# Kernel tuning notes

Measured on AMD Instinct MI355X. Metric: run time of the kernel, lower is better.

## Reference

```python
import jax, jax.numpy as jnp
import numpy as np

B, S, H, D, HID = 2, 4096, 16, 64, 1024
NUM_HASHES, CHUNK, NUM_BUCKETS = 2, 64, 128
N_BEFORE, N_AFTER = 1, 0
HASH_SEED = 0
SELF_MASK_VALUE = -1e5  # fp32 self-mask value from source buffers
EPS = 1e-6


def _look_adjacent(x, n_before, n_after):
    # x: [B,H,C,chunk,...]; concat chunks rolled along chunk axis (2) onto within-chunk axis (3)
    slices = [jnp.roll(x, -i, axis=2) for i in range(-n_before, n_after + 1)]
    return jnp.concatenate(slices, axis=3)


def _hash_vectors(vectors, rotations, num_buckets):
    # vectors: [B,H,S,D]; rotations: [H,D,NUM_HASHES,num_buckets//2] (shared q/k, seed reset in source)
    v = jax.lax.stop_gradient(vectors)  # vectors.detach() in source
    rotated = jnp.einsum('bhsd,hdnr->bhnsr', v, rotations)
    rotated = jnp.concatenate([rotated, -rotated], axis=-1)
    buckets = jnp.argmax(rotated, axis=-1)  # [B,H,NUM_HASHES,S]
    offsets = (jnp.arange(NUM_HASHES) * num_buckets).reshape(1, 1, -1, 1)
    return (buckets + offsets).reshape(vectors.shape[0], H, -1)  # [B,H,NUM_HASHES*S]


def _sorted_and_undo(buckets, seq_len):
    orig = jnp.arange(NUM_HASHES * seq_len) % seq_len
    scaled = seq_len * buckets + orig  # stable within-bucket ordering by position
    sorted_idx = jnp.argsort(scaled, axis=-1)
    undo_idx = jnp.argsort(sorted_idx, axis=-1)  # scatter-inverse of the sort
    return sorted_idx, undo_idx


def _len_and_dim_norm(x):
    var = jnp.mean(x * x, axis=-1, keepdims=True)
    return x * jax.lax.rsqrt(var + EPS) * np.float32(1.0 / np.sqrt(D))


def setup_inputs() -> dict:
    key = jax.random.key(0)
    k1, k2, k3, k4 = jax.random.split(key, 4)
    return {
        'decoder_states': jax.random.normal(k1, (B, S, HID), jnp.float32),
        'hidden_states': jax.random.normal(k2, (B, S, HID), jnp.float32),
        'w_qk': jax.random.normal(k3, (HID, H * D), jnp.float32) / np.float32(np.sqrt(HID)),
        'w_v': jax.random.normal(k4, (HID, H * D), jnp.float32) / np.float32(np.sqrt(HID)),
    }


def reference(decoder_states, hidden_states, w_qk, w_v):
    # projections (bias-free, Reformer-style), split heads -> [B,H,S,D]
    q = (decoder_states @ w_qk).reshape(B, S, H, D).transpose(0, 2, 1, 3)
    k = (hidden_states @ w_qk).reshape(B, S, H, D).transpose(0, 2, 1, 3)
    v = (hidden_states @ w_v).reshape(B, S, H, D).transpose(0, 2, 1, 3)

    rotations = jax.random.normal(jax.random.key(HASH_SEED),
                                  (H, D, NUM_HASHES, NUM_BUCKETS // 2), jnp.float32)
    q_buckets = _hash_vectors(q, rotations, NUM_BUCKETS)
    k_buckets = _hash_vectors(k, rotations, NUM_BUCKETS)
    sorted_q_idx, _ = _sorted_and_undo(q_buckets, S)
    sorted_k_idx, undo_k_idx = _sorted_and_undo(k_buckets, S)
    sorted_q_pos = sorted_q_idx % S
    sorted_k_pos = sorted_k_idx % S

    gather = lambda x, idx: jnp.take_along_axis(x, idx[..., None], axis=2)
    qs = gather(q, sorted_q_pos)  # [B,H,NUM_HASHES*S,D]
    ks = gather(k, sorted_k_pos)
    vs = gather(v, sorted_k_pos)

    n_chunks = NUM_HASHES * S // CHUNK
    to_chunks = lambda x: x.reshape(B, H, n_chunks, CHUNK, D)
    qs, ks, vs = to_chunks(qs), to_chunks(ks), to_chunks(vs)
    ks = _len_and_dim_norm(ks)

    ks = _look_adjacent(ks, N_BEFORE, N_AFTER)  # [B,H,C,2*CHUNK,D]
    vs = _look_adjacent(vs, N_BEFORE, N_AFTER)
    dots = jnp.einsum('bhcqd,bhckd->bhcqk', qs, ks)

    # self-mask: query position == adjacent key position (both from sorted QUERY idx, per source)
    q_idx = sorted_q_pos.reshape(B, H, n_chunks, CHUNK)
    kv_idx = _look_adjacent(q_idx, N_BEFORE, N_AFTER)  # [B,H,C,2*CHUNK]
    self_mask = q_idx[..., :, None] != kv_idx[..., None, :]
    dots = jnp.where(self_mask, dots, SELF_MASK_VALUE)

    logits = jax.nn.logsumexp(dots, axis=-1, keepdims=True)
    probs = jnp.exp(dots - logits)
    out = jnp.einsum('bhcqk,bhckd->bhcqd', probs, vs)

    out = out.reshape(B, H, NUM_HASHES * S, D)
    logits = logits.reshape(B, H, NUM_HASHES * S)
    # ReverseSort uses the KEY undo indices (as in source)
    out = jnp.take_along_axis(out, undo_k_idx[..., None], axis=2)
    logits = jnp.take_along_axis(logits, undo_k_idx, axis=2)

    # merge hash rounds via logsumexp weights (num_hashes > 1 branch)
    out = out.reshape(B, H, NUM_HASHES, S, D)
    logits = logits.reshape(B, H, NUM_HASHES, S, 1)
    w = jnp.exp(logits - jax.nn.logsumexp(logits, axis=2, keepdims=True))
    out = jnp.sum(out * w, axis=2)  # [B,H,S,D]
    return out.transpose(0, 2, 1, 3).reshape(B, S, H * D)
```

## Files before the change

kernel.cpp:

```cpp
#include <hip/hip_runtime.h>
#include <cstdint>
#include <cstddef>

#define BB 2
#define SS 4096
#define HH 16
#define DD 64
#define HID 1024
#define NHASH 2
#define CHUNK 64
#define NBUCK 128
#define NCHUNKS 128
#define NSORT 8192
#define BHN 32

#define KC_BLOCK 288

static constexpr size_t SZ_QKV  = (size_t)BB*HH*SS*DD*4;
static constexpr size_t OFF_Q   = 0;
static constexpr size_t OFF_K   = OFF_Q + SZ_QKV;
static constexpr size_t OFF_V   = OFF_K + SZ_QKV;
static constexpr size_t OFF_ROT = OFF_V + SZ_QKV;
static constexpr size_t OFF_QB  = OFF_ROT + (size_t)131072*4;
static constexpr size_t OFF_KB  = OFF_QB + (size_t)BHN*NSORT*4;
static constexpr size_t OFF_SQ  = OFF_KB + (size_t)BHN*NSORT*4;
static constexpr size_t OFF_SK  = OFF_SQ + (size_t)BHN*NSORT*4;
static constexpr size_t OFF_OUTR= OFF_SK + (size_t)BHN*NSORT*4;
static constexpr size_t OFF_LR  = OFF_OUTR + (size_t)BHN*NSORT*DD*4;
static constexpr size_t OFF_HBF = OFF_LR + (size_t)BHN*NSORT*4;
static constexpr size_t OFF_WBF = OFF_HBF + (size_t)8192*1024*2;
static constexpr size_t WS_REQUIRED = OFF_WBF + (size_t)1024*1024*2;

__device__ __forceinline__ float nofma_mul(float a, float b) {
  float r = a * b;
  asm("" : "+v"(r));
  return r;
}

__device__ __forceinline__ float xla_log1p_f32(float x) {
  float t = nofma_mul(-0.5f, x) + 1.0f;
  float small = nofma_mul(t, x);
  float onep = 1.0f + x;
  float big = (float)log((double)onep);
  return (fabsf(x) < 1e-4f) ? small : big;
}

__device__ __forceinline__ float erfinv_xla_f32(float x) {
  float nxx = -nofma_mul(x, x);
  float w = -xla_log1p_f32(nxx);
  float p;
  if (w < 5.0f) {
    float ww = w - 2.5f;
    p = 2.81022636e-08f;
    p = nofma_mul(p, ww) + 3.43273939e-07f;
    p = nofma_mul(p, ww) + -3.5233877e-06f;
    p = nofma_mul(p, ww) + -4.39150654e-06f;
    p = nofma_mul(p, ww) + 0.00021858087f;
    p = nofma_mul(p, ww) + -0.00125372503f;
    p = nofma_mul(p, ww) + -0.00417768164f;
    p = nofma_mul(p, ww) + 0.246640727f;
    p = nofma_mul(p, ww) + 1.50140941f;
  } else {
    float ww = sqrtf(w) - 3.0f;
    p = -0.000200214257f;
    p = nofma_mul(p, ww) + 0.000100950558f;
    p = nofma_mul(p, ww) + 0.00134934322f;
    p = nofma_mul(p, ww) + -0.00367342844f;
    p = nofma_mul(p, ww) + 0.00573950773f;
    p = nofma_mul(p, ww) + -0.0076224613f;
    p = nofma_mul(p, ww) + 0.00943887047f;
    p = nofma_mul(p, ww) + 1.00167406f;
    p = nofma_mul(p, ww) + 2.83297682f;
  }
  return nofma_mul(p, x);
}

__global__ void gen_rot_kernel(float* __restrict__ rot) {
  unsigned i = blockIdx.x * 256 + threadIdx.x;
  if (i >= 131072u) return;
  unsigned x0 = 0u, x1 = i;
  const unsigned ks2 = 0x1BD11BDAu;
#define TF_ROUND(r) { x0 += x1; x1 = (x1 << r) | (x1 >> (32 - r)); x1 ^= x0; }
  TF_ROUND(13) TF_ROUND(15) TF_ROUND(26) TF_ROUND(6)
              x1 += ks2 + 1u;
  TF_ROUND(17) TF_ROUND(29) TF_ROUND(16) TF_ROUND(24)
   x0 += ks2; x1 += 2u;
  TF_ROUND(13) TF_ROUND(15) TF_ROUND(26) TF_ROUND(6)
              x1 += 3u;
  TF_ROUND(17) TF_ROUND(29) TF_ROUND(16) TF_ROUND(24)
              x1 += ks2 + 4u;
  TF_ROUND(13) TF_ROUND(15) TF_ROUND(26) TF_ROUND(6)
   x0 += ks2; x1 += 5u;
#undef TF_ROUND
  unsigned bits = x0 ^ x1;
  float f = __uint_as_float(0x3f800000u | (bits >> 9)) - 1.0f;
  float u = f * 2.0f - 0.99999994f;
  u = fmaxf(-0.99999994f, u);
  rot[i] = nofma_mul(1.41421356f, erfinv_xla_f32(u));
}

__global__ __launch_bounds__(256) void gemm_kernel(const float* __restrict__ A,
                                                   const float* __restrict__ W,
                                                   float* __restrict__ dst) {
  __shared__ float As[32][132];
  __shared__ float Bs[32][68];
  const int m0 = blockIdx.x * 128;
  const int n0 = blockIdx.y * 64;
  const int tid = threadIdx.x;
  const int tr = tid >> 4, tc = tid & 15;
  float accT[8][4], acc[8][4];
#pragma unroll
  for (int i = 0; i < 8; ++i)
#pragma unroll
    for (int j2 = 0; j2 < 4; ++j2) { accT[i][j2] = 0.f; acc[i][j2] = 0.f; }

  float4 av[4], bv[2];
#pragma unroll
  for (int it = 0; it < 4; ++it) {
    int id = tid + it * 256;
    av[it] = *(const float4*)(A + (size_t)(m0 + (id >> 3)) * 1024 + ((id & 7) << 2));
  }
#pragma unroll
  for (int it = 0; it < 2; ++it) {
    int id = tid + it * 256;
    bv[it] = *(const float4*)(W + (size_t)(id >> 4) * 1024 + n0 + ((id & 15) << 2));
  }
  for (int kk = 0; kk < 1024; kk += 32) {
#pragma unroll
    for (int it = 0; it < 4; ++it) {
      int id = tid + it * 256;
      int m = id >> 3, kq = (id & 7) << 2;
      As[kq + 0][m] = av[it].x;
      As[kq + 1][m] = av[it].y;
      As[kq + 2][m] = av[it].z;
      As[kq + 3][m] = av[it].w;
    }
#pragma unroll
    for (int it = 0; it < 2; ++it) {
      int id = tid + it * 256;
      *(float4*)&Bs[id >> 4][(id & 15) << 2] = bv[it];
    }
    __syncthreads();
    if (kk + 32 < 1024) {
      int kn = kk + 32;
#pragma unroll
      for (int it = 0; it < 4; ++it) {
        int id = tid + it * 256;
        av[it] = *(const float4*)(A + (size_t)(m0 + (id >> 3)) * 1024 + kn + ((id & 7) << 2));
      }
#pragma unroll
      for (int it = 0; it < 2; ++it) {
        int id = tid + it * 256;
        bv[it] = *(const float4*)(W + (size_t)(kn + (id >> 4)) * 1024 + n0 + ((id & 15) << 2));
      }
    }
#pragma unroll
    for (int k = 0; k < 32; ++k) {
      float4 a0 = *(const float4*)&As[k][tr * 8];
      float4 a1 = *(const float4*)&As[k][tr * 8 + 4];
      float4 b0 = *(const float4*)&Bs[k][tc * 4];
      float a[8] = {a0.x, a0.y, a0.z, a0.w, a1.x, a1.y, a1.z, a1.w};
      float b[4] = {b0.x, b0.y, b0.z, b0.w};
#pragma unroll
      for (int i = 0; i < 8; ++i)
#pragma unroll
        for (int j2 = 0; j2 < 4; ++j2)
          acc[i][j2] = fmaf(a[i], b[j2], acc[i][j2]);
    }
    __syncthreads();
    if (((kk + 32) % KC_BLOCK) == 0) {
#pragma unroll
      for (int i = 0; i < 8; ++i)
#pragma unroll
        for (int j2 = 0; j2 < 4; ++j2) { accT[i][j2] += acc[i][j2]; acc[i][j2] = 0.f; }
    }
  }
#pragma unroll
  for (int i = 0; i < 8; ++i)
#pragma unroll
    for (int j2 = 0; j2 < 4; ++j2) accT[i][j2] += acc[i][j2];

  const int h = n0 >> 6;
  const int d = tc << 2;
#pragma unroll
  for (int i = 0; i < 8; ++i) {
    int m = m0 + tr * 8 + i;
    int b = m >> 12, s = m & 4095;
    float4 t = {accT[i][0], accT[i][1], accT[i][2], accT[i][3]};
    *(float4*)(dst + (((size_t)(b * 16 + h) * 4096 + s) << 6) + d) = t;
  }
}

__device__ __forceinline__ unsigned short f2bf(float f) {
  unsigned u = __float_as_uint(f);
  return (unsigned short)((u + 0x7fffu + ((u >> 16) & 1u)) >> 16);
}
__global__ void cast_bf16_kernel(const float* __restrict__ src,
                                 unsigned short* __restrict__ dst, int n4) {
  int i = blockIdx.x * 256 + threadIdx.x;
  if (i >= n4) return;
  float4 v = ((const float4*)src)[i];
  ushort4 o = {f2bf(v.x), f2bf(v.y), f2bf(v.z), f2bf(v.w)};
  ((ushort4*)dst)[i] = o;
}

typedef __attribute__((ext_vector_type(8))) short bf16x8;
typedef __attribute__((ext_vector_type(4))) float f32x4;

__global__ __launch_bounds__(256) void gemm_v_mfma(const unsigned short* __restrict__ Ab,
                                                   const unsigned short* __restrict__ Wb,
                                                   float* __restrict__ dst) {
  __shared__ unsigned short Bt[64][40];
  const int m0 = blockIdx.x * 64;
  const int n0 = blockIdx.y * 64;
  const int tid = threadIdx.x;
  const int w = tid >> 6, l = tid & 63;
  f32x4 acc[4];
#pragma unroll
  for (int fi = 0; fi < 4; ++fi) acc[fi] = {0.f, 0.f, 0.f, 0.f};

  const int arow = m0 + w * 16 + (l & 15);
  const int kgrp = (l >> 4) * 8;
  for (int kk = 0; kk < 1024; kk += 32) {
    {
      int k = tid >> 3, n8 = (tid & 7) * 8;
      bf16x8 v = *(const bf16x8*)(Wb + (size_t)(kk + k) * 1024 + n0 + n8);
#pragma unroll
      for (int i = 0; i < 8; ++i) Bt[n8 + i][k] = (unsigned short)v[i];
    }
    __syncthreads();
    bf16x8 a = *(const bf16x8*)(Ab + (size_t)arow * 1024 + kk + kgrp);
#pragma unroll
    for (int fi = 0; fi < 4; ++fi) {
      bf16x8 b = *(const bf16x8*)(&Bt[fi * 16 + (l & 15)][kgrp]);
      acc[fi] = __builtin_amdgcn_mfma_f32_16x16x32_bf16(a, b, acc[fi], 0, 0, 0);
    }
    __syncthreads();
  }
  const int h = n0 >> 6;
  const int mrow = m0 + w * 16 + (l >> 4) * 4;
#pragma unroll
  for (int fi = 0; fi < 4; ++fi) {
    int d = fi * 16 + (l & 15);
#pragma unroll
    for (int r = 0; r < 4; ++r) {
      int m = mrow + r;
      int b = m >> 12, s = m & 4095;
      dst[(((size_t)(b * 16 + h) * 4096 + s) << 6) + d] = acc[fi][r];
    }
  }
}

__global__ __launch_bounds__(128) void hash_kernel(const float* __restrict__ x,
                                                   const float* __restrict__ rot,
                                                   int* __restrict__ buck) {
  __shared__ float rs[8192];
  const int bh = blockIdx.y;
  const int h = bh & 15;
  const int s0 = blockIdx.x * 128;
  const int tid = threadIdx.x;
  for (int off = tid * 4; off < 8192; off += 512)
    *(float4*)&rs[off] = *(const float4*)(rot + (size_t)h * 8192 + off);
  __syncthreads();
  const int s = s0 + tid;
  const float* xr = x + ((size_t)bh * SS + s) * DD;
  float xv[64];
#pragma unroll
  for (int d4 = 0; d4 < 16; ++d4) {
    float4 t = *(const float4*)(xr + d4 * 4);
    xv[d4 * 4] = t.x; xv[d4 * 4 + 1] = t.y; xv[d4 * 4 + 2] = t.z; xv[d4 * 4 + 3] = t.w;
  }
#pragma unroll
  for (int n = 0; n < 2; ++n) {
    float acc[64];
#pragma unroll
    for (int r = 0; r < 64; ++r) acc[r] = 0.f;
#pragma unroll 2
    for (int d4 = 0; d4 < 16; ++d4) {
#pragma unroll
      for (int dd = 0; dd < 4; ++dd) {
        const float xd = xv[d4 * 4 + dd];
        const float* rp = rs + (d4 * 4 + dd) * 128 + n * 64;
#pragma unroll
        for (int r4 = 0; r4 < 16; ++r4) {
          float4 rv = *(const float4*)(rp + r4 * 4);
          acc[r4 * 4 + 0] = fmaf(xd, rv.x, acc[r4 * 4 + 0]);
          acc[r4 * 4 + 1] = fmaf(xd, rv.y, acc[r4 * 4 + 1]);
          acc[r4 * 4 + 2] = fmaf(xd, rv.z, acc[r4 * 4 + 2]);
          acc[r4 * 4 + 3] = fmaf(xd, rv.w, acc[r4 * 4 + 3]);
        }
      }
    }
    float best = -3.402823466e38f;
    int bi = 0;
#pragma unroll
    for (int idx = 0; idx < 128; ++idx) {
      float val = (idx < 64) ? acc[idx] : -acc[idx - 64];
      if (val > best) { best = val; bi = idx; }
    }
    buck[(size_t)bh * NSORT + n * SS + s] = bi + n * NBUCK;
  }
}

__global__ __launch_bounds__(256) void sort_kernel(const int* __restrict__ buck,
                                                   int* __restrict__ sorted) {
  const int bh = blockIdx.x >> 1;
  const int half = blockIdx.x & 1;
  const int* bk = buck + (size_t)bh * NSORT + half * SS;
  int* out = sorted + (size_t)bh * NSORT + half * SS;
  __shared__ int cnt[64][128];
  __shared__ int bl[SS];
  __shared__ int bbase[128];
  __shared__ int total[128];
  const int tid = threadIdx.x;
  for (int i = tid; i < 64 * 128; i += 256) (&cnt[0][0])[i] = 0;
  __syncthreads();
#pragma unroll
  for (int j = 0; j < 16; ++j) {
    int i = j * 256 + tid;
    int e = bk[i];
    bl[i] = e;
    atomicAdd(&cnt[i >> 6][e & 127], 1);
  }
  __syncthreads();
  if (tid < 128) {
    int s = 0;
#pragma unroll 4
    for (int c = 0; c < 64; ++c) {
      int t = cnt[c][tid];
      cnt[c][tid] = s;
      s += t;
    }
    total[tid] = s;
  }
  __syncthreads();
  if (tid == 0) {
    int s = 0;
#pragma unroll 4
    for (int v = 0; v < 128; ++v) { bbase[v] = s; s += total[v]; }
  }
  __syncthreads();
  if (tid < 64) {
    const int i0 = tid << 6;
    const int orig0 = half * SS + i0;
#pragma unroll 4
    for (int j = 0; j < 64; ++j) {
      int v = bl[i0 + j] & 127;
      int off = cnt[tid][v];
      cnt[tid][v] = off + 1;
      out[bbase[v] + off] = orig0 + j;
    }
  }
}

__global__ void undo_kernel(const int* __restrict__ srt, int* __restrict__ undo) {
  const int bh = blockIdx.x;
  for (int j = threadIdx.x; j < NSORT; j += 256)
    undo[(size_t)bh * NSORT + srt[(size_t)bh * NSORT + j]] = j;
}

__global__ __launch_bounds__(256) void attn_kernel(const float* __restrict__ q,
                                                   const float* __restrict__ k,
                                                   const float* __restrict__ v,
                                                   const int* __restrict__ sq,
                                                   const int* __restrict__ sk,
                                                   float* __restrict__ outr,
                                                   float* __restrict__ lr) {
  const int c = blockIdx.x;
  const int bh = blockIdx.y;
  const int cprev = (c + NCHUNKS - 1) & (NCHUNKS - 1);
  __shared__ float Ks[128][68];
  __shared__ float Vs[128][68];
  __shared__ int qpos[64];
  __shared__ int kvpos[128];
  __shared__ int krow[128];
  __shared__ float kscale[128];
  const int tid = threadIdx.x;
  const int* sqb = sq + (size_t)bh * NSORT;
  const int* skb = sk + (size_t)bh * NSORT;
  if (tid < 64) {
    int sqc = sqb[c * 64 + tid];
    int sqp = sqb[cprev * 64 + tid];
    qpos[tid] = sqc & (SS - 1);
    kvpos[tid] = sqp & (SS - 1);
    kvpos[64 + tid] = sqc & (SS - 1);
    int skc = skb[c * 64 + tid];
    int skp = skb[cprev * 64 + tid];
    krow[tid] = skp & (SS - 1);
    krow[64 + tid] = skc & (SS - 1);
  }
  __syncthreads();
  const float* kb = k + (size_t)bh * SS * DD;
  const float* vb = v + (size_t)bh * SS * DD;
#pragma unroll
  for (int it = 0; it < 8; ++it) {
    int id = tid + it * 256;
    int row = id >> 4, c4 = (id & 15) * 4;
    int srow = krow[row];
    *(float4*)&Ks[row][c4] = *(const float4*)(kb + (size_t)srow * DD + c4);
    *(float4*)&Vs[row][c4] = *(const float4*)(vb + (size_t)srow * DD + c4);
  }
  __syncthreads();
  if (tid < 128) {
    float ss = 0.f;
#pragma unroll
    for (int c4 = 0; c4 < 16; ++c4) {
      float4 t = *(const float4*)&Ks[tid][c4 * 4];
      ss += t.x * t.x + t.y * t.y + t.z * t.z + t.w * t.w;
    }
    kscale[tid] = rsqrtf(ss * (1.f / 64.f) + 1e-6f) * 0.125f;
  }
  __syncthreads();

  const int qi = tid >> 2, g = tid & 3;
  const int qp = qpos[qi];
  const float* qrow = q + ((size_t)bh * SS + qp) * DD;
  float qreg[64];
#pragma unroll
  for (int d4 = 0; d4 < 16; ++d4) {
    float4 t = *(const float4*)(qrow + d4 * 4);
    qreg[d4 * 4] = t.x; qreg[d4 * 4 + 1] = t.y; qreg[d4 * 4 + 2] = t.z; qreg[d4 * 4 + 3] = t.w;
  }
  float dots[32];
#pragma unroll
  for (int j = 0; j < 32; ++j) {
    const int kj = j * 4 + g;
    float acc = 0.f;
#pragma unroll
    for (int d4 = 0; d4 < 16; ++d4) {
      float4 t = *(const float4*)&Ks[kj][d4 * 4];
      acc = fmaf(qreg[d4 * 4 + 0], t.x, acc);
      acc = fmaf(qreg[d4 * 4 + 1], t.y, acc);
      acc = fmaf(qreg[d4 * 4 + 2], t.z, acc);
      acc = fmaf(qreg[d4 * 4 + 3], t.w, acc);
    }
    acc *= kscale[kj];
    if (qp == kvpos[kj]) acc = -1e5f;
    dots[j] = acc;
  }
  float m = dots[0];
#pragma unroll
  for (int j = 1; j < 32; ++j) m = fmaxf(m, dots[j]);
  m = fmaxf(m, __shfl_xor(m, 1));
  m = fmaxf(m, __shfl_xor(m, 2));
  float se = 0.f;
#pragma unroll
  for (int j = 0; j < 32; ++j) { dots[j] = expf(dots[j] - m); se += dots[j]; }
  se += __shfl_xor(se, 1);
  se += __shfl_xor(se, 2);
  const float logit = m + logf(se);
  const float seinv = 1.f / se;
  float o[64];
#pragma unroll
  for (int d = 0; d < 64; ++d) o[d] = 0.f;
#pragma unroll
  for (int j = 0; j < 32; ++j) {
    const int kj = j * 4 + g;
    const float p = dots[j] * seinv;
#pragma unroll
    for (int d4 = 0; d4 < 16; ++d4) {
      float4 t = *(const float4*)&Vs[kj][d4 * 4];
      o[d4 * 4 + 0] = fmaf(p, t.x, o[d4 * 4 + 0]);
      o[d4 * 4 + 1] = fmaf(p, t.y, o[d4 * 4 + 1]);
      o[d4 * 4 + 2] = fmaf(p, t.z, o[d4 * 4 + 2]);
      o[d4 * 4 + 3] = fmaf(p, t.w, o[d4 * 4 + 3]);
    }
  }
#pragma unroll
  for (int d = 0; d < 64; ++d) {
    o[d] += __shfl_xor(o[d], 1);
    o[d] += __shfl_xor(o[d], 2);
  }
  float* orow = outr + ((size_t)bh * NSORT + c * 64 + qi) * DD;
#pragma unroll
  for (int d4 = 0; d4 < 4; ++d4) {
    float4 t = {o[g * 16 + d4 * 4], o[g * 16 + d4 * 4 + 1], o[g * 16 + d4 * 4 + 2], o[g * 16 + d4 * 4 + 3]};
    *(float4*)(orow + g * 16 + d4 * 4) = t;
  }
  if (g == 0) lr[(size_t)bh * NSORT + c * 64 + qi] = logit;
}

__global__ void merge_kernel(const float* __restrict__ outr, const float* __restrict__ lr,
                             const int* __restrict__ undo, float* __restrict__ out) {
  const int idx = blockIdx.x * 256 + threadIdx.x;
  const int d4 = idx & 15;
  const int s = (idx >> 4) & (SS - 1);
  const int bh = idx >> 16;
  const int b = bh >> 4, h = bh & 15;
  const int u0 = undo[(size_t)bh * NSORT + s];
  const int u1 = undo[(size_t)bh * NSORT + SS + s];
  const float l0 = lr[(size_t)bh * NSORT + u0];
  const float l1 = lr[(size_t)bh * NSORT + u1];
  const float m = fmaxf(l0, l1);
  float w0 = expf(l0 - m), w1 = expf(l1 - m);
  const float inv = 1.f / (w0 + w1);
  w0 *= inv; w1 *= inv;
  const float4 r0 = *(const float4*)(outr + ((size_t)bh * NSORT + u0) * DD + d4 * 4);
  const float4 r1 = *(const float4*)(outr + ((size_t)bh * NSORT + u1) * DD + d4 * 4);
  float4 o;
  o.x = w0 * r0.x + w1 * r1.x;
  o.y = w0 * r0.y + w1 * r1.y;
  o.z = w0 * r0.z + w1 * r1.z;
  o.w = w0 * r0.w + w1 * r1.w;
  *(float4*)(out + ((size_t)(b * SS + s) * 1024) + h * 64 + d4 * 4) = o;
}

extern "C" void kernel_launch(void* const* d_in, const int* in_sizes, int n_in,
                              void* d_out, int out_size, void* d_ws, size_t ws_size,
                              hipStream_t stream) {
  if (ws_size < WS_REQUIRED) return;
  const float* dec = (const float*)d_in[0];
  const float* hid = (const float*)d_in[1];
  const float* wqk = (const float*)d_in[2];
  const float* wv  = (const float*)d_in[3];
  float* out = (float*)d_out;
  char* ws = (char*)d_ws;
  float* q    = (float*)(ws + OFF_Q);
  float* kk   = (float*)(ws + OFF_K);
  float* vv   = (float*)(ws + OFF_V);
  float* rotp = (float*)(ws + OFF_ROT);
  int*   qb   = (int*)(ws + OFF_QB);
  int*   kbk  = (int*)(ws + OFF_KB);
  int*   sqi  = (int*)(ws + OFF_SQ);
  int*   ski  = (int*)(ws + OFF_SK);
  float* outr = (float*)(ws + OFF_OUTR);
  float* lrp  = (float*)(ws + OFF_LR);
  unsigned short* hbf = (unsigned short*)(ws + OFF_HBF);
  unsigned short* wbf = (unsigned short*)(ws + OFF_WBF);

  gen_rot_kernel<<<512, 256, 0, stream>>>(rotp);
  cast_bf16_kernel<<<8192, 256, 0, stream>>>(hid, hbf, 8192 * 1024 / 4);
  cast_bf16_kernel<<<1024, 256, 0, stream>>>(wv, wbf, 1024 * 1024 / 4);
  gemm_kernel<<<dim3(64, 16), 256, 0, stream>>>(dec, wqk, q);
  gemm_kernel<<<dim3(64, 16), 256, 0, stream>>>(hid, wqk, kk);
  gemm_v_mfma<<<dim3(128, 16), 256, 0, stream>>>(hbf, wbf, vv);
  hash_kernel<<<dim3(32, 32), 128, 0, stream>>>(q, rotp, qb);
  hash_kernel<<<dim3(32, 32), 128, 0, stream>>>(kk, rotp, kbk);
  sort_kernel<<<64, 256, 0, stream>>>(qb, sqi);
  sort_kernel<<<64, 256, 0, stream>>>(kbk, ski);
  undo_kernel<<<32, 256, 0, stream>>>(ski, qb);
  attn_kernel<<<dim3(128, 32), 256, 0, stream>>>(q, kk, vv, sqi, ski, outr, lrp);
  merge_kernel<<<8192, 256, 0, stream>>>(outr, lrp, qb, out);
}
```

Baseline: 0.9996 ms.

## Rewrite chunked attention with bf16 MFMA for QK^T and PV

The scalar fp32 attention kernel is replaced by one that stages Q, K and transposed V in shared memory as bf16 and computes QK^T and P·V with 16x16x32 bf16 MFMA instructions. Softmax row reductions now run across lanes in the MFMA output layout, and the probabilities go through shared memory as bf16. V is now written as bf16 by the V GEMM, and Q and K get two extra cast kernels. This cuts FP32 ALU work and the bandwidth of the K/V gathers, at the cost of bf16 rounding in the scores, the probabilities and the key norm.

```diff
diff --git a/kernel.cpp b/kernel.cpp
--- a/kernel.cpp
+++ b/kernel.cpp
@@ -29,7 +29,9 @@
 static constexpr size_t OFF_LR  = OFF_OUTR + (size_t)BHN*NSORT*DD*4;
 static constexpr size_t OFF_HBF = OFF_LR + (size_t)BHN*NSORT*4;
 static constexpr size_t OFF_WBF = OFF_HBF + (size_t)8192*1024*2;
-static constexpr size_t WS_REQUIRED = OFF_WBF + (size_t)1024*1024*2;
+static constexpr size_t OFF_QBF = OFF_WBF + (size_t)1024*1024*2;
+static constexpr size_t OFF_KBF = OFF_QBF + (size_t)BHN*SS*DD*2;
+static constexpr size_t WS_REQUIRED = OFF_KBF + (size_t)BHN*SS*DD*2;
 
 __device__ __forceinline__ float nofma_mul(float a, float b) {
   float r = a * b;
@@ -209,7 +211,7 @@
 
 __global__ __launch_bounds__(256) void gemm_v_mfma(const unsigned short* __restrict__ Ab,
                                                    const unsigned short* __restrict__ Wb,
-                                                   float* __restrict__ dst) {
+                                                   unsigned short* __restrict__ dst) {
   __shared__ unsigned short Bt[64][40];
   const int m0 = blockIdx.x * 64;
   const int n0 = blockIdx.y * 64;
@@ -246,7 +248,7 @@
     for (int r = 0; r < 4; ++r) {
       int m = mrow + r;
       int b = m >> 12, s = m & 4095;
-      dst[(((size_t)(b * 16 + h) * 4096 + s) << 6) + d] = acc[fi][r];
+      dst[(((size_t)(b * 16 + h) * 4096 + s) << 6) + d] = f2bf(acc[fi][r]);
     }
   }
 }
@@ -359,18 +361,17 @@
     undo[(size_t)bh * NSORT + srt[(size_t)bh * NSORT + j]] = j;
 }
 
-__global__ __launch_bounds__(256) void attn_kernel(const float* __restrict__ q,
-                                                   const float* __restrict__ k,
-                                                   const float* __restrict__ v,
-                                                   const int* __restrict__ sq,
-                                                   const int* __restrict__ sk,
-                                                   float* __restrict__ outr,
-                                                   float* __restrict__ lr) {
-  const int c = blockIdx.x;
-  const int bh = blockIdx.y;
+__global__ __launch_bounds__(256) void attn_mfma_kernel(
+    const unsigned short* __restrict__ qb16, const unsigned short* __restrict__ kb16,
+    const unsigned short* __restrict__ vb16,
+    const int* __restrict__ sq, const int* __restrict__ sk,
+    float* __restrict__ outr, float* __restrict__ lr) {
+  const int c = blockIdx.x, bh = blockIdx.y;
   const int cprev = (c + NCHUNKS - 1) & (NCHUNKS - 1);
-  __shared__ float Ks[128][68];
-  __shared__ float Vs[128][68];
+  __shared__ unsigned short Qs[64][80];
+  __shared__ unsigned short Ks[128][80];
+  __shared__ unsigned short Vt[64][136];
+  __shared__ unsigned short Ps[64][136];
   __shared__ int qpos[64];
   __shared__ int kvpos[128];
   __shared__ int krow[128];
@@ -384,100 +385,122 @@
     qpos[tid] = sqc & (SS - 1);
     kvpos[tid] = sqp & (SS - 1);
     kvpos[64 + tid] = sqc & (SS - 1);
-    int skc = skb[c * 64 + tid];
-    int skp = skb[cprev * 64 + tid];
-    krow[tid] = skp & (SS - 1);
-    krow[64 + tid] = skc & (SS - 1);
-  }
-  __syncthreads();
-  const float* kb = k + (size_t)bh * SS * DD;
-  const float* vb = v + (size_t)bh * SS * DD;
-#pragma unroll
-  for (int it = 0; it < 8; ++it) {
+    krow[tid] = skb[cprev * 64 + tid] & (SS - 1);
+    krow[64 + tid] = skb[c * 64 + tid] & (SS - 1);
+  }
+  __syncthreads();
+  const unsigned short* kbase = kb16 + (size_t)bh * SS * DD;
+  const unsigned short* vbase = vb16 + (size_t)bh * SS * DD;
+  const unsigned short* qbase = qb16 + (size_t)bh * SS * DD;
+#pragma unroll
+  for (int it = 0; it < 4; ++it) {
     int id = tid + it * 256;
-    int row = id >> 4, c4 = (id & 15) * 4;
-    int srow = krow[row];
-    *(float4*)&Ks[row][c4] = *(const float4*)(kb + (size_t)srow * DD + c4);
-    *(float4*)&Vs[row][c4] = *(const float4*)(vb + (size_t)srow * DD + c4);
+    int row = id >> 3, seg = id & 7;
+    *(bf16x8*)&Ks[row][seg * 8] = *(const bf16x8*)(kbase + (size_t)krow[row] * DD + seg * 8);
+  }
+#pragma unroll
+  for (int it = 0; it < 2; ++it) {
+    int id = tid + it * 256;
+    int row = id >> 3, seg = id & 7;
+    *(bf16x8*)&Qs[row][seg * 8] = *(const bf16x8*)(qbase + (size_t)qpos[row] * DD + seg * 8);
+  }
+#pragma unroll
+  for (int it = 0; it < 4; ++it) {
+    int id = tid + it * 256;
+    int col = id & 127, dg = id >> 7;
+    bf16x8 v = *(const bf16x8*)(vbase + (size_t)krow[col] * DD + dg * 8);
+#pragma unroll
+    for (int i = 0; i < 8; ++i) Vt[dg * 8 + i][col] = (unsigned short)v[i];
   }
   __syncthreads();
   if (tid < 128) {
     float ss = 0.f;
 #pragma unroll
-    for (int c4 = 0; c4 < 16; ++c4) {
-      float4 t = *(const float4*)&Ks[tid][c4 * 4];
-      ss += t.x * t.x + t.y * t.y + t.z * t.z + t.w * t.w;
+    for (int seg = 0; seg < 8; ++seg) {
+      bf16x8 t = *(const bf16x8*)&Ks[tid][seg * 8];
+#pragma unroll
+      for (int i = 0; i < 8; ++i) {
+        float f = __uint_as_float(((unsigned)(unsigned short)t[i]) << 16);
+        ss = fmaf(f, f, ss);
+      }
     }
     kscale[tid] = rsqrtf(ss * (1.f / 64.f) + 1e-6f) * 0.125f;
   }
   __syncthreads();
 
-  const int qi = tid >> 2, g = tid & 3;
-  const int qp = qpos[qi];
-  const float* qrow = q + ((size_t)bh * SS + qp) * DD;
-  float qreg[64];
-#pragma unroll
-  for (int d4 = 0; d4 < 16; ++d4) {
-    float4 t = *(const float4*)(qrow + d4 * 4);
-    qreg[d4 * 4] = t.x; qreg[d4 * 4 + 1] = t.y; qreg[d4 * 4 + 2] = t.z; qreg[d4 * 4 + 3] = t.w;
-  }
-  float dots[32];
-#pragma unroll
-  for (int j = 0; j < 32; ++j) {
-    const int kj = j * 4 + g;
-    float acc = 0.f;
-#pragma unroll
-    for (int d4 = 0; d4 < 16; ++d4) {
-      float4 t = *(const float4*)&Ks[kj][d4 * 4];
-      acc = fmaf(qreg[d4 * 4 + 0], t.x, acc);
-      acc = fmaf(qreg[d4 * 4 + 1], t.y, acc);
-      acc = fmaf(qreg[d4 * 4 + 2], t.z, acc);
-      acc = fmaf(qreg[d4 * 4 + 3], t.w, acc);
-    }
-    acc *= kscale[kj];
-    if (qp == kvpos[kj]) acc = -1e5f;
-    dots[j] = acc;
-  }
-  float m = dots[0];
-#pragma unroll
-  for (int j = 1; j < 32; ++j) m = fmaxf(m, dots[j]);
-  m = fmaxf(m, __shfl_xor(m, 1));
-  m = fmaxf(m, __shfl_xor(m, 2));
-  float se = 0.f;
-#pragma unroll
-  for (int j = 0; j < 32; ++j) { dots[j] = expf(dots[j] - m); se += dots[j]; }
-  se += __shfl_xor(se, 1);
-  se += __shfl_xor(se, 2);
-  const float logit = m + logf(se);
-  const float seinv = 1.f / se;
-  float o[64];
-#pragma unroll
-  for (int d = 0; d < 64; ++d) o[d] = 0.f;
-#pragma unroll
-  for (int j = 0; j < 32; ++j) {
-    const int kj = j * 4 + g;
-    const float p = dots[j] * seinv;
-#pragma unroll
-    for (int d4 = 0; d4 < 16; ++d4) {
-      float4 t = *(const float4*)&Vs[kj][d4 * 4];
-      o[d4 * 4 + 0] = fmaf(p, t.x, o[d4 * 4 + 0]);
-      o[d4 * 4 + 1] = fmaf(p, t.y, o[d4 * 4 + 1]);
-      o[d4 * 4 + 2] = fmaf(p, t.z, o[d4 * 4 + 2]);
-      o[d4 * 4 + 3] = fmaf(p, t.w, o[d4 * 4 + 3]);
-    }
-  }
-#pragma unroll
-  for (int d = 0; d < 64; ++d) {
-    o[d] += __shfl_xor(o[d], 1);
-    o[d] += __shfl_xor(o[d], 2);
-  }
-  float* orow = outr + ((size_t)bh * NSORT + c * 64 + qi) * DD;
-#pragma unroll
-  for (int d4 = 0; d4 < 4; ++d4) {
-    float4 t = {o[g * 16 + d4 * 4], o[g * 16 + d4 * 4 + 1], o[g * 16 + d4 * 4 + 2], o[g * 16 + d4 * 4 + 3]};
-    *(float4*)(orow + g * 16 + d4 * 4) = t;
-  }
-  if (g == 0) lr[(size_t)bh * NSORT + c * 64 + qi] = logit;
+  const int w = tid >> 6, l = tid & 63;
+  const int lc = l & 15, lg = l >> 4;
+  bf16x8 a0 = *(const bf16x8*)&Qs[w * 16 + lc][lg * 8];
+  bf16x8 a1 = *(const bf16x8*)&Qs[w * 16 + lc][32 + lg * 8];
+  f32x4 accs[8];
+#pragma unroll
+  for (int fi = 0; fi < 8; ++fi) {
+    f32x4 acc = {0.f, 0.f, 0.f, 0.f};
+    bf16x8 b0 = *(const bf16x8*)&Ks[fi * 16 + lc][lg * 8];
+    bf16x8 b1 = *(const bf16x8*)&Ks[fi * 16 + lc][32 + lg * 8];
+    acc = __builtin_amdgcn_mfma_f32_16x16x32_bf16(a0, b0, acc, 0, 0, 0);
+    acc = __builtin_amdgcn_mfma_f32_16x16x32_bf16(a1, b1, acc, 0, 0, 0);
+    accs[fi] = acc;
+  }
+  float kcs[8]; int kvp[8];
+#pragma unroll
+  for (int fi = 0; fi < 8; ++fi) { kcs[fi] = kscale[fi * 16 + lc]; kvp[fi] = kvpos[fi * 16 + lc]; }
+  float ex[8][4], logit_r[4], seinv_r[4];
+#pragma unroll
+  for (int r = 0; r < 4; ++r) {
+    const int qp = qpos[w * 16 + lg * 4 + r];
+    float mr = -3.402823466e38f;
+#pragma unroll
+    for (int fi = 0; fi < 8; ++fi) {
+      float d = accs[fi][r] * kcs[fi];
+      if (qp == kvp[fi]) d = -1e5f;
+      ex[fi][r] = d;
+      mr = fmaxf(mr, d);
+    }
+    mr = fmaxf(mr, __shfl_xor(mr, 1));
+    mr = fmaxf(mr, __shfl_xor(mr, 2));
+    mr = fmaxf(mr, __shfl_xor(mr, 4));
+    mr = fmaxf(mr, __shfl_xor(mr, 8));
+    float s = 0.f;
+#pragma unroll
+    for (int fi = 0; fi < 8; ++fi) { float e = expf(ex[fi][r] - mr); ex[fi][r] = e; s += e; }
+    s += __shfl_xor(s, 1);
+    s += __shfl_xor(s, 2);
+    s += __shfl_xor(s, 4);
+    s += __shfl_xor(s, 8);
+    logit_r[r] = mr + logf(s);
+    seinv_r[r] = 1.f / s;
+  }
+#pragma unroll
+  for (int r = 0; r < 4; ++r) {
+    int row = w * 16 + lg * 4 + r;
+#pragma unroll
+    for (int fi = 0; fi < 8; ++fi)
+      Ps[row][fi * 16 + lc] = f2bf(ex[fi][r]);
+    if (lc == 0) lr[(size_t)bh * NSORT + c * 64 + row] = logit_r[r];
+  }
+  __syncthreads();
+  f32x4 acco[4];
+#pragma unroll
+  for (int fi2 = 0; fi2 < 4; ++fi2) acco[fi2] = {0.f, 0.f, 0.f, 0.f};
+#pragma unroll
+  for (int kg = 0; kg < 4; ++kg) {
+    bf16x8 a = *(const bf16x8*)&Ps[w * 16 + lc][kg * 32 + lg * 8];
+#pragma unroll
+    for (int fi2 = 0; fi2 < 4; ++fi2) {
+      bf16x8 b = *(const bf16x8*)&Vt[fi2 * 16 + lc][kg * 32 + lg * 8];
+      acco[fi2] = __builtin_amdgcn_mfma_f32_16x16x32_bf16(a, b, acco[fi2], 0, 0, 0);
+    }
+  }
+#pragma unroll
+  for (int fi2 = 0; fi2 < 4; ++fi2) {
+    int d = fi2 * 16 + lc;
+#pragma unroll
+    for (int r = 0; r < 4; ++r) {
+      int row = w * 16 + lg * 4 + r;
+      outr[((size_t)bh * NSORT + c * 64 + row) * DD + d] = acco[fi2][r] * seinv_r[r];
+    }
+  }
 }
 
 __global__ void merge_kernel(const float* __restrict__ outr, const float* __restrict__ lr,
@@ -517,7 +540,7 @@
   char* ws = (char*)d_ws;
   float* q    = (float*)(ws + OFF_Q);
   float* kk   = (float*)(ws + OFF_K);
-  float* vv   = (float*)(ws + OFF_V);
+  unsigned short* vbf = (unsigned short*)(ws + OFF_V);
   float* rotp = (float*)(ws + OFF_ROT);
   int*   qb   = (int*)(ws + OFF_QB);
   int*   kbk  = (int*)(ws + OFF_KB);
@@ -527,18 +550,22 @@
   float* lrp  = (float*)(ws + OFF_LR);
   unsigned short* hbf = (unsigned short*)(ws + OFF_HBF);
   unsigned short* wbf = (unsigned short*)(ws + OFF_WBF);
+  unsigned short* qbf = (unsigned short*)(ws + OFF_QBF);
+  unsigned short* kbf = (unsigned short*)(ws + OFF_KBF);
 
   gen_rot_kernel<<<512, 256, 0, stream>>>(rotp);
   cast_bf16_kernel<<<8192, 256, 0, stream>>>(hid, hbf, 8192 * 1024 / 4);
   cast_bf16_kernel<<<1024, 256, 0, stream>>>(wv, wbf, 1024 * 1024 / 4);
   gemm_kernel<<<dim3(64, 16), 256, 0, stream>>>(dec, wqk, q);
   gemm_kernel<<<dim3(64, 16), 256, 0, stream>>>(hid, wqk, kk);
-  gemm_v_mfma<<<dim3(128, 16), 256, 0, stream>>>(hbf, wbf, vv);
+  gemm_v_mfma<<<dim3(128, 16), 256, 0, stream>>>(hbf, wbf, vbf);
   hash_kernel<<<dim3(32, 32), 128, 0, stream>>>(q, rotp, qb);
   hash_kernel<<<dim3(32, 32), 128, 0, stream>>>(kk, rotp, kbk);
+  cast_bf16_kernel<<<8192, 256, 0, stream>>>(q, qbf, 8192 * 1024 / 4);
+  cast_bf16_kernel<<<8192, 256, 0, stream>>>(kk, kbf, 8192 * 1024 / 4);
   sort_kernel<<<64, 256, 0, stream>>>(qb, sqi);
   sort_kernel<<<64, 256, 0, stream>>>(kbk, ski);
   undo_kernel<<<32, 256, 0, stream>>>(ski, qb);
-  attn_kernel<<<dim3(128, 32), 256, 0, stream>>>(q, kk, vv, sqi, ski, outr, lrp);
+  attn_mfma_kernel<<<dim3(128, 32), 256, 0, stream>>>(qbf, kbf, vbf, sqi, ski, outr, lrp);
   merge_kernel<<<8192, 256, 0, stream>>>(outr, lrp, qb, out);
 }
```

Measured after the change: 826.5 us. -17.3%, faster.
